# Performance work log

Measured on AMD Instinct MI355X. Metric: run time of the kernel, lower is better.

Reference implementation:

```python
import jax, jax.numpy as jnp
import numpy as np

N_NODES = 100000
N_EDGES = 3200000
D = 128
BN_EPS = 1e-5


def setup_inputs() -> dict:
    key = jax.random.key(0)
    k1, k2, k3, k4 = jax.random.split(key, 4)
    x = jax.random.normal(k1, (N_NODES, D), dtype=jnp.float32)
    edge_index = jax.random.randint(k2, (2, N_EDGES), 0, N_NODES, dtype=jnp.int64)
    # GCNConv linear weight, torch nn.Linear convention: [out_dim, in_dim]
    W = jax.random.normal(k3, (D, D), dtype=jnp.float32) * (1.0 / np.sqrt(D))
    # BatchNorm1d affine params
    gamma = jnp.ones((D,), dtype=jnp.float32) + 0.1 * jax.random.normal(k4, (D,), dtype=jnp.float32)
    beta = jnp.zeros((D,), dtype=jnp.float32)
    return {"x": x, "edge_index": edge_index, "W": W, "gamma": gamma, "beta": beta}


def reference(x, edge_index, W, gamma, beta):
    # GCNConv(bias=False, add_self_loops=False), then BN (batch stats), ReLU, skip-add.
    src, dst = edge_index[0], edge_index[1]
    n = x.shape[0]

    # linear transform: [N, D_out]
    h = x @ W.T

    # symmetric GCN normalization: deg over destination, norm = d^-1/2[src]*d^-1/2[dst]
    ones = jnp.ones((src.shape[0],), dtype=x.dtype)
    deg = jax.ops.segment_sum(ones, dst, num_segments=n)
    dinv = jnp.where(deg > 0, jax.lax.rsqrt(jnp.maximum(deg, 1.0)), 0.0)
    norm = dinv[src] * dinv[dst]  # [E]

    # gather-message-scatter: [E, D] -> [N, D]
    msg = h[src] * norm[:, None]
    agg = jax.ops.segment_sum(msg, dst, num_segments=n)

    # BatchNorm1d in training mode (batch statistics, biased variance)
    mean = jnp.mean(agg, axis=0)
    var = jnp.mean(jnp.square(agg - mean), axis=0)
    bn = (agg - mean) * jax.lax.rsqrt(var + BN_EPS) * gamma + beta

    # ReLU + residual skip (dims match)
    out = jax.nn.relu(bn) + x
    return out
```

## Files before the change

### kernel.cpp

```cpp
#include <hip/hip_runtime.h>
#include <hip/hip_bf16.h>
#include <cstdint>
#include <cstddef>

#define D 128
#define SBBITS 10
#define NSB 128
#define TILE 4096
#define BINT 512
#define NSLOT 64

typedef __attribute__((ext_vector_type(8))) short short8;
typedef __attribute__((ext_vector_type(4))) float f32x4;

__device__ __forceinline__ unsigned short f2bf(float f) {
    union { float f; unsigned u; } v; v.f = f;
    unsigned r = v.u + 0x7FFF + ((v.u >> 16) & 1);
    return (unsigned short)(r >> 16);
}
__device__ __forceinline__ float bflo(unsigned p) {
    union { unsigned u; float f; } v; v.u = p << 16; return v.f;
}
__device__ __forceinline__ float bfhi(unsigned p) {
    union { unsigned u; float f; } v; v.u = p & 0xFFFF0000u; return v.f;
}

__global__ __launch_bounds__(256) void k_prep(const unsigned* __restrict__ ei, int E,
                                              int* __restrict__ flag,
                                              const float* __restrict__ W,
                                              unsigned short* __restrict__ Wbf,
                                              int* __restrict__ g_sbcnt,
                                              float* __restrict__ part2) {
    int t = threadIdx.x, b = blockIdx.x;
    int i = b * 256 + t;
    if (i < D * D) Wbf[i] = f2bf(W[i]);
    part2[i] = 0.f;
    if (b == 0 && t == 0) {
        int n = E < 256 ? E : 256;
        int allz = 1;
        for (int k = 0; k < n; ++k) {
            if (ei[2 * k + 1] != 0u) { allz = 0; break; }
        }
        *flag = allz;
    }
    if (b == 63 && t < NSB) g_sbcnt[t] = 0;
}

__global__ __launch_bounds__(256) void k_gemm(const float* __restrict__ x,
                                              const unsigned short* __restrict__ Wbf,
                                              unsigned short* __restrict__ h, int M) {
    int wave = threadIdx.x >> 6, lane = threadIdx.x & 63;
    int m0 = blockIdx.x * 64 + wave * 16;
    int lr = lane & 15;
    int lg = lane >> 4;
    f32x4 acc[8];
#pragma unroll
    for (int i = 0; i < 8; ++i) acc[i] = (f32x4){0.f, 0.f, 0.f, 0.f};

    int row = m0 + lr;
    int rowc = row < M ? row : M - 1;
    const float* xr = x + (size_t)rowc * D;

#pragma unroll
    for (int ks = 0; ks < 4; ++ks) {
        int k0 = ks * 32 + lg * 8;
        float4 a0 = *(const float4*)(xr + k0);
        float4 a1 = *(const float4*)(xr + k0 + 4);
        short8 af;
        af[0] = (short)f2bf(a0.x); af[1] = (short)f2bf(a0.y);
        af[2] = (short)f2bf(a0.z); af[3] = (short)f2bf(a0.w);
        af[4] = (short)f2bf(a1.x); af[5] = (short)f2bf(a1.y);
        af[6] = (short)f2bf(a1.z); af[7] = (short)f2bf(a1.w);
#pragma unroll
        for (int nt = 0; nt < 8; ++nt) {
            short8 bf = *(const short8*)(Wbf + (size_t)(nt * 16 + lr) * D + k0);
            acc[nt] = __builtin_amdgcn_mfma_f32_16x16x32_bf16(af, bf, acc[nt], 0, 0, 0);
        }
    }
#pragma unroll
    for (int nt = 0; nt < 8; ++nt) {
#pragma unroll
        for (int r = 0; r < 4; ++r) {
            int rr = m0 + lg * 4 + r;
            if (rr < M) h[(size_t)rr * D + nt * 16 + lr] = f2bf(acc[nt][r]);
        }
    }
}

__global__ __launch_bounds__(BINT) void k_bin(const int* __restrict__ ei, int E,
                                              const int* __restrict__ flagp,
                                              int* __restrict__ g_sbcnt,
                                              unsigned* __restrict__ binned, int C2) {
    __shared__ unsigned stage[TILE];
    __shared__ unsigned char ssb[TILE];
    __shared__ int hcnt[NSB], hoff[NSB], lcur[NSB], gbase[NSB];
    int f64 = *flagp;
    int t = threadIdx.x;
    int base = blockIdx.x * TILE;
    int cnt = E - base; if (cnt > TILE) cnt = TILE;

    if (t < NSB) hcnt[t] = 0;
    __syncthreads();

    unsigned ent[8]; int esb[8];
#pragma unroll
    for (int j = 0; j < 8; ++j) {
        int idx = j * BINT + t;
        esb[j] = -1;
        if (idx < cnt) {
            int e = base + idx;
            int s, d;
            if (f64) { s = ei[2 * e]; d = ei[2 * (E + e)]; }
            else     { s = ei[e];     d = ei[E + e]; }
            esb[j] = d >> SBBITS;
            ent[j] = (unsigned)s | ((unsigned)(d & ((1 << SBBITS) - 1)) << 17);
            atomicAdd(&hcnt[esb[j]], 1);
        }
    }
    __syncthreads();
    if (t < NSB) hoff[t] = hcnt[t];
    __syncthreads();
#pragma unroll
    for (int off = 1; off < NSB; off <<= 1) {
        int a = (t < NSB && t >= off) ? hoff[t - off] : 0;
        __syncthreads();
        if (t < NSB) hoff[t] += a;
        __syncthreads();
    }
    if (t < NSB) {
        int ex = hoff[t] - hcnt[t];
        lcur[t] = ex;
        hoff[t] = ex;
        gbase[t] = (hcnt[t] > 0) ? atomicAdd(&g_sbcnt[t], hcnt[t]) : 0;
    }
    __syncthreads();
#pragma unroll
    for (int j = 0; j < 8; ++j) {
        if (esb[j] >= 0) {
            int p = atomicAdd(&lcur[esb[j]], 1);
            stage[p] = ent[j];
            ssb[p] = (unsigned char)esb[j];
        }
    }
    __syncthreads();
    for (int i = t; i < cnt; i += BINT) {
        int sb = ssb[i];
        int pos = gbase[sb] + (i - hoff[sb]);
        if (pos < C2) binned[(size_t)sb * C2 + pos] = stage[i];
    }
}

__global__ __launch_bounds__(1024) void k_fill2(const unsigned* __restrict__ binned, int C2,
                                                const int* __restrict__ g_sbcnt,
                                                int2* __restrict__ ronode,
                                                float* __restrict__ dinv,
                                                int* __restrict__ csrc, int N) {
    __shared__ int deg[1024];
    __shared__ int scn[1024];
    __shared__ int cur[1024];
    int b = blockIdx.x, t = threadIdx.x;
    int cnt = g_sbcnt[b]; if (cnt > C2) cnt = C2;
    const unsigned* ent = binned + (size_t)b * C2;

    deg[t] = 0;
    __syncthreads();
    for (int i = t; i < cnt; i += 1024) atomicAdd(&deg[ent[i] >> 17], 1);
    __syncthreads();
    scn[t] = deg[t];
    __syncthreads();
    for (int off = 1; off < 1024; off <<= 1) {
        int a = (t >= off) ? scn[t - off] : 0;
        __syncthreads();
        scn[t] += a;
        __syncthreads();
    }
    int ex = scn[t] - deg[t];
    cur[t] = ex;
    int node = (b << SBBITS) + t;
    if (node < N) {
        ronode[node] = make_int2(b * C2 + ex, deg[t]);
        dinv[node] = deg[t] > 0 ? rsqrtf((float)deg[t]) : 0.0f;
    }
    __syncthreads();
    for (int i = t; i < cnt; i += 1024) {
        unsigned e = ent[i];
        int pos = atomicAdd(&cur[e >> 17], 1);
        csrc[b * C2 + pos] = (int)(e & 0x1FFFF);
    }
}

__global__ __launch_bounds__(256) void k_agg(const unsigned long long* __restrict__ h,
                                             const int* __restrict__ csrc,
                                             const int2* __restrict__ ronode,
                                             const float* __restrict__ dinv,
                                             float4* __restrict__ out,
                                             float* __restrict__ part2, int N) {
    __shared__ float ssum[128], ssq[128];
    int t = threadIdx.x;
    int wave = t >> 6, lane = t & 63;
    int node = blockIdx.x * 4 + wave;
    int half = lane >> 5, lq = lane & 31;
    if (t < 128) { ssum[t] = 0.f; ssq[t] = 0.f; }
    __syncthreads();

    float v0 = 0.f, v1 = 0.f, v2 = 0.f, v3 = 0.f;
    if (node < N) {
        int2 ro = ronode[node];
        int beg = ro.x, end = ro.x + ro.y;
        float a0 = 0.f, a1 = 0.f, a2 = 0.f, a3 = 0.f;
        int i = beg;
        for (; i + 16 <= end; i += 16) {
#pragma unroll
            for (int p = 0; p < 8; ++p) {
                int e = i + 2 * p + half;
                int s = csrc[e];
                float w = dinv[s];
                unsigned long long pk = h[(size_t)s * 32 + lq];
                unsigned lo = (unsigned)pk, hi = (unsigned)(pk >> 32);
                a0 += w * bflo(lo); a1 += w * bfhi(lo);
                a2 += w * bflo(hi); a3 += w * bfhi(hi);
            }
        }
        for (; i + 2 <= end; i += 2) {
            int e = i + half;
            int s = csrc[e];
            float w = dinv[s];
            unsigned long long pk = h[(size_t)s * 32 + lq];
            unsigned lo = (unsigned)pk, hi = (unsigned)(pk >> 32);
            a0 += w * bflo(lo); a1 += w * bfhi(lo);
            a2 += w * bflo(hi); a3 += w * bfhi(hi);
        }
        if (i < end) {
            int s = csrc[i];
            float w = half ? 0.f : dinv[s];
            unsigned long long pk = h[(size_t)s * 32 + lq];
            unsigned lo = (unsigned)pk, hi = (unsigned)(pk >> 32);
            a0 += w * bflo(lo); a1 += w * bfhi(lo);
            a2 += w * bflo(hi); a3 += w * bfhi(hi);
        }
        a0 += __shfl_xor(a0, 32);
        a1 += __shfl_xor(a1, 32);
        a2 += __shfl_xor(a2, 32);
        a3 += __shfl_xor(a3, 32);
        float sd = dinv[node];
        v0 = a0 * sd; v1 = a1 * sd; v2 = a2 * sd; v3 = a3 * sd;
        if (half == 0) {
            out[(size_t)node * 32 + lq] = make_float4(v0, v1, v2, v3);
            int c = lq * 4;
            atomicAdd(&ssum[c],     v0); atomicAdd(&ssq[c],     v0 * v0);
            atomicAdd(&ssum[c + 1], v1); atomicAdd(&ssq[c + 1], v1 * v1);
            atomicAdd(&ssum[c + 2], v2); atomicAdd(&ssq[c + 2], v2 * v2);
            atomicAdd(&ssum[c + 3], v3); atomicAdd(&ssq[c + 3], v3 * v3);
        }
    }
    __syncthreads();
    int slot = blockIdx.x & (NSLOT - 1);
    if (t < 128)            atomicAdd(&part2[slot * 256 + t],       ssum[t]);
    else if (t < 256)       atomicAdd(&part2[slot * 256 + t],       ssq[t - 128]);
}

__global__ void k_params(const float* __restrict__ part2, const float* __restrict__ gamma,
                         const float* __restrict__ beta, float* __restrict__ params, int N) {
    int t = threadIdx.x;
    float a = 0.f;
    for (int s = 0; s < NSLOT; ++s) a += part2[s * 256 + t];
    __shared__ float sh[256];
    sh[t] = a;
    __syncthreads();
    if (t < 128) {
        float mean = sh[t] / (float)N;
        float var = sh[128 + t] / (float)N - mean * mean;
        var = var > 0.f ? var : 0.f;
        float sc = gamma[t] * rsqrtf(var + 1e-5f);
        params[t] = sc;
        params[128 + t] = beta[t] - mean * sc;
    }
}

__global__ __launch_bounds__(256) void k_final(float4* __restrict__ out,
                                               const float4* __restrict__ x,
                                               const float* __restrict__ params, int n4) {
    const float4* p4 = (const float4*)params;
    for (int i = blockIdx.x * 256 + threadIdx.x; i < n4; i += gridDim.x * 256) {
        int c = i & 31;
        float4 s = p4[c], b = p4[32 + c];
        float4 v = out[i], xv = x[i];
        float4 r;
        r.x = fmaxf(v.x * s.x + b.x, 0.f) + xv.x;
        r.y = fmaxf(v.y * s.y + b.y, 0.f) + xv.y;
        r.z = fmaxf(v.z * s.z + b.z, 0.f) + xv.z;
        r.w = fmaxf(v.w * s.w + b.w, 0.f) + xv.w;
        out[i] = r;
    }
}

extern "C" void kernel_launch(void* const* d_in, const int* in_sizes, int n_in,
                              void* d_out, int out_size, void* d_ws, size_t ws_size,
                              hipStream_t stream) {
    const float* x     = (const float*)d_in[0];
    const int*   ei    = (const int*)d_in[1];
    const float* W     = (const float*)d_in[2];
    const float* gamma = (const float*)d_in[3];
    const float* beta  = (const float*)d_in[4];

    int N = in_sizes[0] / D;
    int E = in_sizes[1] / 2;
    int NSBu = (N + (1 << SBBITS) - 1) >> SBBITS;
    int avg = (E + NSBu - 1) / NSBu;
    int C2 = ((avg + 4096 + 63) / 64) * 64;

    char* ws = (char*)d_ws;
    size_t off = 0;
    auto alloc = [&](size_t bytes) { size_t o = off; off = (off + bytes + 255) & ~(size_t)255; return o; };

    unsigned short* h    = (unsigned short*)(ws + alloc((size_t)N * D * 2));
    int*      csrc   = (int*)     (ws + alloc((size_t)NSBu * C2 * 4));
    unsigned* binned = (unsigned*)(ws + alloc((size_t)NSBu * C2 * 4));
    int*      g_sbcnt= (int*)     (ws + alloc((size_t)NSB * 4));
    float*    dinv   = (float*)   (ws + alloc((size_t)N * 4));
    int2*     ronode = (int2*)    (ws + alloc((size_t)N * 8));
    float*    part2  = (float*)   (ws + alloc((size_t)NSLOT * 256 * 4));
    float*    params = (float*)   (ws + alloc(256 * 4));
    int*      flagp  = (int*)     (ws + alloc(4));
    unsigned short* Wbf = (unsigned short*)(ws + alloc((size_t)D * D * 2));

    k_prep<<<64, 256, 0, stream>>>((const unsigned*)ei, E, flagp, W, Wbf, g_sbcnt, part2);
    k_gemm<<<(N + 63) / 64, 256, 0, stream>>>(x, Wbf, h, N);
    k_bin<<<(E + TILE - 1) / TILE, BINT, 0, stream>>>(ei, E, flagp, g_sbcnt, binned, C2);
    k_fill2<<<NSBu, 1024, 0, stream>>>(binned, C2, g_sbcnt, ronode, dinv, csrc, N);
    k_agg<<<(N + 3) / 4, 256, 0, stream>>>((const unsigned long long*)h, csrc, ronode, dinv,
                                           (float4*)d_out, part2, N);
    k_params<<<1, 256, 0, stream>>>(part2, gamma, beta, params, N);
    k_final<<<2048, 256, 0, stream>>>((float4*)d_out, (const float4*)x, params,
                                      (N * D) / 4);
}
```

Before: 422.2 us.

## Persistent grid for aggregation, LDS-staged GEMM input, int2 edge loads

The aggregation kernel moves to a fixed 2048-block grid-stride loop over nodes. Each thread keeps its BN sum and sum-of-squares in registers, so there is one set of shared and global atomics per block instead of one per node. The GEMM stages the x tile into LDS as bf16 with coalesced loads before the MFMA loop, rather than each lane converting its own strided rows. The binning kernel reads int64 edge indices as int2 loads. The persistent grid cuts block launch and atomic overhead but may balance the load across nodes of varying degree less well.

```diff
diff --git a/kernel.cpp b/kernel.cpp
--- a/kernel.cpp
+++ b/kernel.cpp
@@ -9,6 +9,7 @@
 #define TILE 4096
 #define BINT 512
 #define NSLOT 64
+#define AGGB 2048
 
 typedef __attribute__((ext_vector_type(8))) short short8;
 typedef __attribute__((ext_vector_type(4))) float f32x4;
@@ -49,34 +50,40 @@
 __global__ __launch_bounds__(256) void k_gemm(const float* __restrict__ x,
                                               const unsigned short* __restrict__ Wbf,
                                               unsigned short* __restrict__ h, int M) {
-    int wave = threadIdx.x >> 6, lane = threadIdx.x & 63;
-    int m0 = blockIdx.x * 64 + wave * 16;
-    int lr = lane & 15;
-    int lg = lane >> 4;
+    __shared__ unsigned short sx[64 * 136];
+    int t = threadIdx.x;
+    int base = blockIdx.x * 64;
+
+#pragma unroll
+    for (int j = 0; j < 8; ++j) {
+        int idx = j * 256 + t;
+        int row = idx >> 5, c4 = (idx & 31) * 4;
+        int gr = base + row;
+        float4 v = (gr < M) ? *(const float4*)(x + (size_t)gr * D + c4)
+                            : make_float4(0.f, 0.f, 0.f, 0.f);
+        unsigned short* dst = &sx[row * 136 + c4];
+        dst[0] = f2bf(v.x); dst[1] = f2bf(v.y); dst[2] = f2bf(v.z); dst[3] = f2bf(v.w);
+    }
+    __syncthreads();
+
+    int wave = t >> 6, lane = t & 63;
+    int lr = lane & 15, lg = lane >> 4;
+    int lrow = wave * 16 + lr;
     f32x4 acc[8];
 #pragma unroll
     for (int i = 0; i < 8; ++i) acc[i] = (f32x4){0.f, 0.f, 0.f, 0.f};
-
-    int row = m0 + lr;
-    int rowc = row < M ? row : M - 1;
-    const float* xr = x + (size_t)rowc * D;
 
 #pragma unroll
     for (int ks = 0; ks < 4; ++ks) {
         int k0 = ks * 32 + lg * 8;
-        float4 a0 = *(const float4*)(xr + k0);
-        float4 a1 = *(const float4*)(xr + k0 + 4);
-        short8 af;
-        af[0] = (short)f2bf(a0.x); af[1] = (short)f2bf(a0.y);
-        af[2] = (short)f2bf(a0.z); af[3] = (short)f2bf(a0.w);
-        af[4] = (short)f2bf(a1.x); af[5] = (short)f2bf(a1.y);
-        af[6] = (short)f2bf(a1.z); af[7] = (short)f2bf(a1.w);
+        short8 af = *(const short8*)(&sx[lrow * 136 + k0]);
 #pragma unroll
         for (int nt = 0; nt < 8; ++nt) {
             short8 bf = *(const short8*)(Wbf + (size_t)(nt * 16 + lr) * D + k0);
             acc[nt] = __builtin_amdgcn_mfma_f32_16x16x32_bf16(af, bf, acc[nt], 0, 0, 0);
         }
     }
+    int m0 = base + wave * 16;
 #pragma unroll
     for (int nt = 0; nt < 8; ++nt) {
 #pragma unroll
@@ -110,8 +117,13 @@
         if (idx < cnt) {
             int e = base + idx;
             int s, d;
-            if (f64) { s = ei[2 * e]; d = ei[2 * (E + e)]; }
-            else     { s = ei[e];     d = ei[E + e]; }
+            if (f64) {
+                s = ((const int2*)ei)[e].x;
+                d = ((const int2*)ei)[E + e].x;
+            } else {
+                s = ei[e];
+                d = ei[E + e];
+            }
             esb[j] = d >> SBBITS;
             ent[j] = (unsigned)s | ((unsigned)(d & ((1 << SBBITS) - 1)) << 17);
             atomicAdd(&hcnt[esb[j]], 1);
@@ -198,13 +210,13 @@
     __shared__ float ssum[128], ssq[128];
     int t = threadIdx.x;
     int wave = t >> 6, lane = t & 63;
-    int node = blockIdx.x * 4 + wave;
     int half = lane >> 5, lq = lane & 31;
     if (t < 128) { ssum[t] = 0.f; ssq[t] = 0.f; }
-    __syncthreads();
-
-    float v0 = 0.f, v1 = 0.f, v2 = 0.f, v3 = 0.f;
-    if (node < N) {
+
+    float ps0 = 0.f, ps1 = 0.f, ps2 = 0.f, ps3 = 0.f;
+    float pq0 = 0.f, pq1 = 0.f, pq2 = 0.f, pq3 = 0.f;
+
+    for (int node = blockIdx.x * 4 + wave; node < N; node += AGGB * 4) {
         int2 ro = ronode[node];
         int beg = ro.x, end = ro.x + ro.y;
         float a0 = 0.f, a1 = 0.f, a2 = 0.f, a3 = 0.f;
@@ -243,20 +255,25 @@
         a2 += __shfl_xor(a2, 32);
         a3 += __shfl_xor(a3, 32);
         float sd = dinv[node];
-        v0 = a0 * sd; v1 = a1 * sd; v2 = a2 * sd; v3 = a3 * sd;
+        float v0 = a0 * sd, v1 = a1 * sd, v2 = a2 * sd, v3 = a3 * sd;
         if (half == 0) {
             out[(size_t)node * 32 + lq] = make_float4(v0, v1, v2, v3);
-            int c = lq * 4;
-            atomicAdd(&ssum[c],     v0); atomicAdd(&ssq[c],     v0 * v0);
-            atomicAdd(&ssum[c + 1], v1); atomicAdd(&ssq[c + 1], v1 * v1);
-            atomicAdd(&ssum[c + 2], v2); atomicAdd(&ssq[c + 2], v2 * v2);
-            atomicAdd(&ssum[c + 3], v3); atomicAdd(&ssq[c + 3], v3 * v3);
-        }
+            ps0 += v0; ps1 += v1; ps2 += v2; ps3 += v3;
+            pq0 += v0 * v0; pq1 += v1 * v1; pq2 += v2 * v2; pq3 += v3 * v3;
+        }
+    }
+    __syncthreads();
+    if (half == 0) {
+        int c = lq * 4;
+        atomicAdd(&ssum[c],     ps0); atomicAdd(&ssq[c],     pq0);
+        atomicAdd(&ssum[c + 1], ps1); atomicAdd(&ssq[c + 1], pq1);
+        atomicAdd(&ssum[c + 2], ps2); atomicAdd(&ssq[c + 2], pq2);
+        atomicAdd(&ssum[c + 3], ps3); atomicAdd(&ssq[c + 3], pq3);
     }
     __syncthreads();
     int slot = blockIdx.x & (NSLOT - 1);
-    if (t < 128)            atomicAdd(&part2[slot * 256 + t],       ssum[t]);
-    else if (t < 256)       atomicAdd(&part2[slot * 256 + t],       ssq[t - 128]);
+    if (t < 128)       atomicAdd(&part2[slot * 256 + t], ssum[t]);
+    else if (t < 256)  atomicAdd(&part2[slot * 256 + t], ssq[t - 128]);
 }
 
 __global__ void k_params(const float* __restrict__ part2, const float* __restrict__ gamma,
@@ -328,8 +345,8 @@
     k_gemm<<<(N + 63) / 64, 256, 0, stream>>>(x, Wbf, h, N);
     k_bin<<<(E + TILE - 1) / TILE, BINT, 0, stream>>>(ei, E, flagp, g_sbcnt, binned, C2);
     k_fill2<<<NSBu, 1024, 0, stream>>>(binned, C2, g_sbcnt, ronode, dinv, csrc, N);
-    k_agg<<<(N + 3) / 4, 256, 0, stream>>>((const unsigned long long*)h, csrc, ronode, dinv,
-                                           (float4*)d_out, part2, N);
+    k_agg<<<AGGB, 256, 0, stream>>>((const unsigned long long*)h, csrc, ronode, dinv,
+                                    (float4*)d_out, part2, N);
     k_params<<<1, 256, 0, stream>>>(part2, gamma, beta, params, N);
     k_final<<<2048, 256, 0, stream>>>((float4*)d_out, (const float4*)x, params,
                                       (N * D) / 4);
```

Result: faster. 396.7 us (-6.0%).
